# Kernel optimization log

Hardware: AMD Instinct MI355X
Metric: run time of the kernel (lower is better)

The kernel has to match this reference:

```python
import jax, jax.numpy as jnp
import numpy as np


def setup_inputs() -> dict:
    key = jax.random.key(0)
    ks = jax.random.split(key, 7)
    B, IN, OUT, G = 8192, 2048, 2048, 4
    s_i = 1.0 / np.sqrt(IN)
    s_h = 1.0 / np.sqrt(OUT)
    return {
        "x": jax.random.normal(ks[0], (B, IN), jnp.float32),
        "prev_h": jax.random.normal(ks[1], (B, OUT), jnp.float32),
        "prev_c": jax.random.normal(ks[2], (B, OUT), jnp.float32),
        "Wi": jax.random.normal(ks[3], (G, IN, OUT), jnp.float32) * s_i,
        "Wh": jax.random.normal(ks[4], (G, OUT, OUT), jnp.float32) * s_h,
        "bi": jax.random.normal(ks[5], (G, OUT), jnp.float32) * s_i,
        "bh": jax.random.normal(ks[6], (G, OUT), jnp.float32) * s_h,
    }


def reference(x, prev_h, prev_c, Wi, Wh, bi, bh):
    # Two fused GEMMs replacing 8 per-gate Linears (gate order: in, forget, in2, out)
    # gates: [B, 4, OUT]
    gates = (jnp.einsum("bi,gio->bgo", x, Wi) + bi[None]
             + jnp.einsum("bh,gho->bgo", prev_h, Wh) + bh[None])
    in_gate = jax.nn.sigmoid(gates[:, 0])
    forget_gate = jax.nn.sigmoid(gates[:, 1])
    in_gate2 = jax.nn.sigmoid(gates[:, 2])
    out_gate = jax.nn.sigmoid(gates[:, 3])
    next_c = forget_gate * prev_c + in_gate * in_gate2
    # NOTE: faithful to source: out_gate + tanh(next_c) (addition, not multiply)
    next_h = out_gate + jnp.tanh(next_c)
    return next_h, next_c
```

## Files before the change

kernel.cpp:

```cpp
#include <hip/hip_runtime.h>
#include <stdint.h>


#define SZ_ELEMS 16777216
#define HALF_OUT 16777216

typedef __attribute__((ext_vector_type(8))) short bf16x8;
typedef __attribute__((ext_vector_type(4))) float f32x4;
typedef __attribute__((ext_vector_type(8))) unsigned short u16x8;

__device__ __forceinline__ unsigned short f2bf(float f) {
  unsigned int u = __float_as_uint(f);
  u += 0x7FFFu + ((u >> 16) & 1u);
  return (unsigned short)(u >> 16);
}

__device__ __forceinline__ void async16(const void* g, void* l) {
  __builtin_amdgcn_global_load_lds(
      (const __attribute__((address_space(1))) void*)g,
      (__attribute__((address_space(3))) void*)l, 16, 0, 0);
}

__device__ __forceinline__ float sigm(float x) { return 1.f / (1.f + __expf(-x)); }

__global__ void cvt_bf16_kernel(const float* __restrict__ src,
                                unsigned short* __restrict__ dst, int n4) {
  int i = blockIdx.x * blockDim.x + threadIdx.x;
  int stride = gridDim.x * blockDim.x;
  for (; i < n4; i += stride) {
    float4 v = reinterpret_cast<const float4*>(src)[i];
    ushort4 o;
    o.x = f2bf(v.x); o.y = f2bf(v.y); o.z = f2bf(v.z); o.w = f2bf(v.w);
    reinterpret_cast<ushort4*>(dst)[i] = o;
  }
}

__global__ void transpose_w_kernel(const float* __restrict__ Wi, const float* __restrict__ Wh,
                                   unsigned short* __restrict__ Wit, unsigned short* __restrict__ Wht) {
  __shared__ float tile[64][65];
  const int tk = blockIdx.x, to = blockIdx.y, gz = blockIdx.z;
  const float* W = (gz < 4 ? Wi : Wh) + (size_t)(gz & 3) * 4194304;
  unsigned short* Wt = (gz < 4 ? Wit : Wht) + (size_t)(gz & 3) * 4194304;
  const int t = threadIdx.x;
  const int o = t & 63, kr = t >> 6;
#pragma unroll
  for (int p = 0; p < 16; ++p) {
    int k = p * 4 + kr;
    tile[k][o] = W[(size_t)(tk * 64 + k) * 2048 + to * 64 + o];
  }
  __syncthreads();
#pragma unroll
  for (int p = 0; p < 2; ++p) {
    int idx = p * 256 + t;
    int orow = idx >> 3, k0 = (idx & 7) * 8;
    u16x8 v;
#pragma unroll
    for (int i = 0; i < 8; ++i) v[i] = f2bf(tile[k0 + i][orow]);
    *reinterpret_cast<u16x8*>(&Wt[(size_t)(to * 64 + orow) * 2048 + tk * 64 + k0]) = v;
  }
}

__global__ __launch_bounds__(512, 2) void lstm_gemm_kernel(
    const unsigned short* __restrict__ xb, const unsigned short* __restrict__ hb,
    const unsigned short* __restrict__ wit, const unsigned short* __restrict__ wht,
    const float* __restrict__ bi, const float* __restrict__ bh,
    const float* __restrict__ prev_c, float* __restrict__ out) {
  __shared__ char lds[131072];

  const int tid = threadIdx.x;
  const int wave = tid >> 6, lane = tid & 63;
  const int wm = wave >> 2, wn = wave & 3;
  const int bm = blockIdx.x;
  const int bo = blockIdx.y;

  int aoff[4], boff[4];
#pragma unroll
  for (int j = 0; j < 4; ++j) {
    int L = j * 8192 + tid * 16;
    int row = L >> 7, c = L & 127;
    aoff[j] = row * 4096 + (c ^ ((row & 7) << 4));
    boff[j] = (row >> 6) * 8388608 + (row & 63) * 4096 + (c ^ ((row & 7) << 4));
  }
  const int ldst = tid * 16;

  const char* aB0 = (const char*)xb + (size_t)bm * 1048576;
  const char* aB1 = (const char*)hb + (size_t)bm * 1048576;
  const char* bB0 = (const char*)wit + (size_t)bo * 262144;
  const char* bB1 = (const char*)wht + (size_t)bo * 262144;

  auto stage = [&](int s, int buf) {
    const char* ab; const char* bb;
    if (s < 32) { ab = aB0 + s * 128;        bb = bB0 + s * 128; }
    else        { ab = aB1 + (s - 32) * 128; bb = bB1 + (s - 32) * 128; }
    char* l = lds + buf * 65536;
#pragma unroll
    for (int j = 0; j < 4; ++j) async16(ab + aoff[j], l + j * 8192 + ldst);
#pragma unroll
    for (int j = 0; j < 4; ++j) async16(bb + boff[j], l + 32768 + j * 8192 + ldst);
  };

  f32x4 acc[8][4];
  const f32x4 zero = {0.f, 0.f, 0.f, 0.f};
#pragma unroll
  for (int mf = 0; mf < 8; ++mf)
#pragma unroll
    for (int nf = 0; nf < 4; ++nf) acc[mf][nf] = zero;

  const int kwin = (lane >> 4) << 4;
  const int swz  = (lane & 7) << 4;
  int aro[8], bro[4];
#pragma unroll
  for (int mf = 0; mf < 8; ++mf) aro[mf] = (wm * 128 + mf * 16 + (lane & 15)) * 128;
#pragma unroll
  for (int nf = 0; nf < 4; ++nf) bro[nf] = 32768 + (nf * 64 + wn * 16 + (lane & 15)) * 128;

  auto compute = [&](int buf) {
    const char* l = lds + buf * 65536;
#pragma unroll
    for (int ks = 0; ks < 2; ++ks) {
      const int kb = (ks * 64 + kwin) ^ swz;
      bf16x8 afr[8];
#pragma unroll
      for (int mf = 0; mf < 8; ++mf) afr[mf] = *(const bf16x8*)(l + aro[mf] + kb);
#pragma unroll
      for (int nf = 0; nf < 4; ++nf) {
        bf16x8 bfr = *(const bf16x8*)(l + bro[nf] + kb);
#pragma unroll
        for (int mf = 0; mf < 8; ++mf)
          acc[mf][nf] = __builtin_amdgcn_mfma_f32_16x16x32_bf16(afr[mf], bfr, acc[mf][nf], 0, 0, 0);
      }
    }
  };

  stage(0, 0);
  for (int t = 0; t < 63; ++t) {
    asm volatile("" ::: "memory");
    __builtin_amdgcn_s_barrier();
    asm volatile("" ::: "memory");
    stage(t + 1, (t + 1) & 1);
    asm volatile("s_waitcnt vmcnt(8)" ::: "memory");
    __builtin_amdgcn_s_barrier();
    asm volatile("" ::: "memory");
    __builtin_amdgcn_s_setprio(1);
    compute(t & 1);
    __builtin_amdgcn_s_setprio(0);
  }
  asm volatile("" ::: "memory");
  __builtin_amdgcn_s_barrier();
  asm volatile("s_waitcnt vmcnt(0)" ::: "memory");
  __builtin_amdgcn_s_barrier();
  asm volatile("" ::: "memory");
  __builtin_amdgcn_s_setprio(1);
  compute(1);
  __builtin_amdgcn_s_setprio(0);

  const int col = lane & 15, rg = lane >> 4;
  const int o = bo * 64 + wn * 16 + col;
  float bs[4];
#pragma unroll
  for (int g = 0; g < 4; ++g) bs[g] = bi[g * 2048 + o] + bh[g * 2048 + o];
#pragma unroll
  for (int mf = 0; mf < 8; ++mf) {
    int bbase = bm * 256 + wm * 128 + mf * 16 + rg * 4;
#pragma unroll
    for (int r = 0; r < 4; ++r) {
      int b = bbase + r;
      float gi = sigm(acc[mf][0][r] + bs[0]);
      float gf = sigm(acc[mf][1][r] + bs[1]);
      float g2 = sigm(acc[mf][2][r] + bs[2]);
      float go = sigm(acc[mf][3][r] + bs[3]);
      float c = prev_c[(size_t)b * 2048 + o];
      float nc = gf * c + gi * g2;
      float e = __expf(2.f * nc);
      float nh = go + (e - 1.f) / (e + 1.f);
      out[(size_t)b * 2048 + o] = nh;
      out[(size_t)HALF_OUT + (size_t)b * 2048 + o] = nc;
    }
  }
}

extern "C" void kernel_launch(void* const* d_in, const int* in_sizes, int n_in,
                              void* d_out, int out_size, void* d_ws, size_t ws_size,
                              hipStream_t stream) {
  const float* x  = (const float*)d_in[0];
  const float* ph = (const float*)d_in[1];
  const float* pc = (const float*)d_in[2];
  const float* Wi = (const float*)d_in[3];
  const float* Wh = (const float*)d_in[4];
  const float* bi = (const float*)d_in[5];
  const float* bh = (const float*)d_in[6];
  float* out = (float*)d_out;

  if (ws_size < (size_t)4 * SZ_ELEMS * sizeof(unsigned short)) return;
  unsigned short* xb  = (unsigned short*)d_ws;
  unsigned short* hb  = xb + SZ_ELEMS;
  unsigned short* wit = hb + SZ_ELEMS;
  unsigned short* wht = wit + SZ_ELEMS;

  cvt_bf16_kernel<<<2048, 256, 0, stream>>>(x, xb, 4194304);
  cvt_bf16_kernel<<<2048, 256, 0, stream>>>(ph, hb, 4194304);
  transpose_w_kernel<<<dim3(32, 32, 8), 256, 0, stream>>>(Wi, Wh, wit, wht);
  lstm_gemm_kernel<<<dim3(32, 32), 512, 0, stream>>>(xb, hb, wit, wht, bi, bh, pc, out);
}
```

Measured before the change: 556.7 us.

## Interleave half-tile async loads with quadrant MFMA phases and swizzle block order

Rewrites the GEMM main loop into an 8-phase ping-pong schedule. Each stage's A and B loads are split into halves and issued between quadrant MFMA groups, with LDS fragment reads done just in time and explicit waitcnt/barrier control. This aims to overlap global-to-LDS traffic and LDS reads with matrix math instead of loading a whole stage and then computing. The grid also becomes 1D with a remapped block order for better L2 reuse across XCDs. The cost is many more barriers per K step and tight hand-tuned counter waits that could be fragile.

```diff
diff --git a/kernel.cpp b/kernel.cpp
--- a/kernel.cpp
+++ b/kernel.cpp
@@ -60,6 +60,13 @@
   }
 }
 
+#define FENCE asm volatile("" ::: "memory")
+#define BARRIER do { FENCE; __builtin_amdgcn_s_barrier(); FENCE; } while (0)
+#define LGKM0 asm volatile("s_waitcnt lgkmcnt(0)" ::: "memory")
+#define LGKM8 asm volatile("s_waitcnt lgkmcnt(8)" ::: "memory")
+#define VMC6  asm volatile("s_waitcnt vmcnt(6)" ::: "memory")
+#define VMC0  asm volatile("s_waitcnt vmcnt(0)" ::: "memory")
+
 __global__ __launch_bounds__(512, 2) void lstm_gemm_kernel(
     const unsigned short* __restrict__ xb, const unsigned short* __restrict__ hb,
     const unsigned short* __restrict__ wit, const unsigned short* __restrict__ wht,
@@ -70,33 +77,47 @@
   const int tid = threadIdx.x;
   const int wave = tid >> 6, lane = tid & 63;
   const int wm = wave >> 2, wn = wave & 3;
-  const int bm = blockIdx.x;
-  const int bo = blockIdx.y;
-
-  int aoff[4], boff[4];
-#pragma unroll
-  for (int j = 0; j < 4; ++j) {
-    int L = j * 8192 + tid * 16;
-    int row = L >> 7, c = L & 127;
-    aoff[j] = row * 4096 + (c ^ ((row & 7) << 4));
-    boff[j] = (row >> 6) * 8388608 + (row & 63) * 4096 + (c ^ ((row & 7) << 4));
-  }
-  const int ldst = tid * 16;
-
-  const char* aB0 = (const char*)xb + (size_t)bm * 1048576;
-  const char* aB1 = (const char*)hb + (size_t)bm * 1048576;
-  const char* bB0 = (const char*)wit + (size_t)bo * 262144;
-  const char* bB1 = (const char*)wht + (size_t)bo * 262144;
-
-  auto stage = [&](int s, int buf) {
-    const char* ab; const char* bb;
-    if (s < 32) { ab = aB0 + s * 128;        bb = bB0 + s * 128; }
-    else        { ab = aB1 + (s - 32) * 128; bb = bB1 + (s - 32) * 128; }
-    char* l = lds + buf * 65536;
-#pragma unroll
-    for (int j = 0; j < 4; ++j) async16(ab + aoff[j], l + j * 8192 + ldst);
-#pragma unroll
-    for (int j = 0; j < 4; ++j) async16(bb + boff[j], l + 32768 + j * 8192 + ldst);
+  const int flat = blockIdx.x;
+  const int swz = (flat & 7) * 128 + (flat >> 3);
+  const int bm = swz & 31, bo = swz >> 5;
+
+  const int kwin = (lane >> 4) << 4;
+  const int fswz = (lane & 7) << 4;
+  int aro[8], bro[4];
+#pragma unroll
+  for (int mf = 0; mf < 8; ++mf) aro[mf] = (wm * 128 + mf * 16 + (lane & 15)) * 128;
+#pragma unroll
+  for (int nf = 0; nf < 4; ++nf) bro[nf] = 32768 + (nf * 64 + wn * 16 + (lane & 15)) * 128;
+
+  const int L0 = tid * 16;
+  int agoff[2][2], bgoff[2][2];
+#pragma unroll
+  for (int h = 0; h < 2; ++h)
+#pragma unroll
+    for (int j = 0; j < 2; ++j) {
+      int L = j * 8192 + L0;
+      int row = h * 128 + (L >> 7);
+      int c = (L & 127) ^ ((row & 7) << 4);
+      agoff[h][j] = row * 4096 + c;
+      int g = row >> 6, orow = row & 63;
+      bgoff[h][j] = g * 8388608 + orow * 4096 + c;
+    }
+  const char* pxa = (const char*)xb + (size_t)bm * 1048576;
+  const char* pha = (const char*)hb + (size_t)bm * 1048576;
+  const char* pwi = (const char*)wit + (size_t)bo * 262144;
+  const char* pwh = (const char*)wht + (size_t)bo * 262144;
+
+  auto stageA = [&](int t, int h, int buf) {
+    const char* base = (t < 32) ? (pxa + t * 128) : (pha + (t - 32) * 128);
+    char* d = lds + buf * 65536 + h * 16384 + L0;
+    async16(base + agoff[h][0], d);
+    async16(base + agoff[h][1], d + 8192);
+  };
+  auto stageB = [&](int t, int h, int buf) {
+    const char* base = (t < 32) ? (pwi + t * 128) : (pwh + (t - 32) * 128);
+    char* d = lds + buf * 65536 + 32768 + h * 16384 + L0;
+    async16(base + bgoff[h][0], d);
+    async16(base + bgoff[h][1], d + 8192);
   };
 
   f32x4 acc[8][4];
@@ -106,53 +127,63 @@
 #pragma unroll
     for (int nf = 0; nf < 4; ++nf) acc[mf][nf] = zero;
 
-  const int kwin = (lane >> 4) << 4;
-  const int swz  = (lane & 7) << 4;
-  int aro[8], bro[4];
-#pragma unroll
-  for (int mf = 0; mf < 8; ++mf) aro[mf] = (wm * 128 + mf * 16 + (lane & 15)) * 128;
-#pragma unroll
-  for (int nf = 0; nf < 4; ++nf) bro[nf] = 32768 + (nf * 64 + wn * 16 + (lane & 15)) * 128;
-
-  auto compute = [&](int buf) {
+  bf16x8 afr[4][2];
+  bf16x8 bfr[4][2];
+
+  auto loadA = [&](int buf, int mh) {
     const char* l = lds + buf * 65536;
 #pragma unroll
-    for (int ks = 0; ks < 2; ++ks) {
-      const int kb = (ks * 64 + kwin) ^ swz;
-      bf16x8 afr[8];
-#pragma unroll
-      for (int mf = 0; mf < 8; ++mf) afr[mf] = *(const bf16x8*)(l + aro[mf] + kb);
-#pragma unroll
-      for (int nf = 0; nf < 4; ++nf) {
-        bf16x8 bfr = *(const bf16x8*)(l + bro[nf] + kb);
-#pragma unroll
-        for (int mf = 0; mf < 8; ++mf)
-          acc[mf][nf] = __builtin_amdgcn_mfma_f32_16x16x32_bf16(afr[mf], bfr, acc[mf][nf], 0, 0, 0);
-      }
-    }
-  };
-
-  stage(0, 0);
-  for (int t = 0; t < 63; ++t) {
-    asm volatile("" ::: "memory");
-    __builtin_amdgcn_s_barrier();
-    asm volatile("" ::: "memory");
-    stage(t + 1, (t + 1) & 1);
-    asm volatile("s_waitcnt vmcnt(8)" ::: "memory");
-    __builtin_amdgcn_s_barrier();
-    asm volatile("" ::: "memory");
+    for (int m = 0; m < 4; ++m)
+#pragma unroll
+      for (int ks = 0; ks < 2; ++ks)
+        afr[m][ks] = *(const bf16x8*)(l + aro[mh * 4 + m] + ((ks * 64 + kwin) ^ fswz));
+  };
+  auto loadB = [&](int buf, int nh) {
+    const char* l = lds + buf * 65536;
+#pragma unroll
+    for (int n = 0; n < 2; ++n)
+#pragma unroll
+      for (int ks = 0; ks < 2; ++ks)
+        bfr[nh * 2 + n][ks] = *(const bf16x8*)(l + bro[nh * 2 + n] + ((ks * 64 + kwin) ^ fswz));
+  };
+  auto MF16 = [&](int mh, int nh) {
     __builtin_amdgcn_s_setprio(1);
-    compute(t & 1);
+#pragma unroll
+    for (int ks = 0; ks < 2; ++ks)
+#pragma unroll
+      for (int n = 0; n < 2; ++n)
+#pragma unroll
+        for (int m = 0; m < 4; ++m)
+          acc[mh * 4 + m][nh * 2 + n] = __builtin_amdgcn_mfma_f32_16x16x32_bf16(
+              afr[m][ks], bfr[nh * 2 + n][ks], acc[mh * 4 + m][nh * 2 + n], 0, 0, 0);
     __builtin_amdgcn_s_setprio(0);
-  }
-  asm volatile("" ::: "memory");
-  __builtin_amdgcn_s_barrier();
-  asm volatile("s_waitcnt vmcnt(0)" ::: "memory");
-  __builtin_amdgcn_s_barrier();
-  asm volatile("" ::: "memory");
-  __builtin_amdgcn_s_setprio(1);
-  compute(1);
-  __builtin_amdgcn_s_setprio(0);
+  };
+
+  stageB(0, 0, 0); stageB(0, 1, 0); stageA(0, 0, 0); stageA(0, 1, 0);
+  stageB(1, 0, 1); stageB(1, 1, 1); stageA(1, 0, 1);
+  VMC6;
+  BARRIER;
+
+  for (int i = 0; i < 31; ++i) {
+    const int t1 = 2 * i + 1, t2 = 2 * i + 2, t3 = 2 * i + 3;
+    loadA(0, 0); loadB(0, 0); stageA(t1, 1, 1); LGKM8; BARRIER; LGKM0; MF16(0, 0); BARRIER;
+    loadB(0, 1); stageB(t2, 0, 0); BARRIER; LGKM0; MF16(0, 1); BARRIER;
+    loadA(0, 1); stageB(t2, 1, 0); BARRIER; LGKM0; MF16(1, 0); BARRIER;
+    stageA(t2, 0, 0); BARRIER; MF16(1, 1); VMC6; BARRIER;
+    loadA(1, 0); loadB(1, 0); stageA(t2, 1, 0); LGKM8; BARRIER; LGKM0; MF16(0, 0); BARRIER;
+    loadB(1, 1); stageB(t3, 0, 1); BARRIER; LGKM0; MF16(0, 1); BARRIER;
+    loadA(1, 1); stageB(t3, 1, 1); BARRIER; LGKM0; MF16(1, 0); BARRIER;
+    stageA(t3, 0, 1); BARRIER; MF16(1, 1); VMC6; BARRIER;
+  }
+
+  loadA(0, 0); loadB(0, 0); stageA(63, 1, 1); LGKM8; BARRIER; LGKM0; MF16(0, 0); BARRIER;
+  loadB(0, 1); BARRIER; LGKM0; MF16(0, 1); BARRIER;
+  loadA(0, 1); BARRIER; LGKM0; MF16(1, 0); BARRIER;
+  BARRIER; MF16(1, 1); VMC0; BARRIER;
+  loadA(1, 0); loadB(1, 0); LGKM8; BARRIER; LGKM0; MF16(0, 0); BARRIER;
+  loadB(1, 1); BARRIER; LGKM0; MF16(0, 1); BARRIER;
+  loadA(1, 1); BARRIER; LGKM0; MF16(1, 0); BARRIER;
+  MF16(1, 1);
 
   const int col = lane & 15, rg = lane >> 4;
   const int o = bo * 64 + wn * 16 + col;
@@ -200,5 +231,5 @@
   cvt_bf16_kernel<<<2048, 256, 0, stream>>>(x, xb, 4194304);
   cvt_bf16_kernel<<<2048, 256, 0, stream>>>(ph, hb, 4194304);
   transpose_w_kernel<<<dim3(32, 32, 8), 256, 0, stream>>>(Wi, Wh, wit, wht);
-  lstm_gemm_kernel<<<dim3(32, 32), 512, 0, stream>>>(xb, hb, wit, wht, bi, bh, pc, out);
-}
+  lstm_gemm_kernel<<<dim3(1024), 512, 0, stream>>>(xb, hb, wit, wht, bi, bh, pc, out);
+}
```

Result: no change. 547.2 us (-1.7%).
